# Optimization experiments

Hardware: AMD Instinct MI355X
Metric: run time of the kernel (lower is better)

The kernel has to match this reference:

```python
import jax, jax.numpy as jnp
import numpy as np

N_NODES = 50000
N_EDGES = 800000
K_HOPS = 3


def setup_inputs() -> dict:
    key = jax.random.key(0)
    ks = jax.random.split(key, 8)
    x = jax.random.normal(ks[0], (N_NODES, 56), dtype=jnp.float32)
    edge_index = jax.random.randint(ks[1], (2, N_EDGES), 0, N_NODES, dtype=jnp.int64)
    def glorot(k, shape):
        fan_in, fan_out = shape
        s = (6.0 / (fan_in + fan_out)) ** 0.5
        return jax.random.uniform(k, shape, jnp.float32, -s, s)
    return {
        "x": x,
        "edge_index": edge_index,
        "W1": glorot(ks[2], (56, 64)), "b1": jnp.zeros((64,), jnp.float32),
        "W2": glorot(ks[3], (64, 64)), "b2": jnp.zeros((64,), jnp.float32),
        "W3": glorot(ks[4], (64, 64)), "b3": jnp.zeros((64,), jnp.float32),
        "W4": glorot(ks[5], (64, 256)), "b4": jnp.zeros((256,), jnp.float32),
    }


def _gcn_norm(edge_index, num_nodes, dtype):
    # add self loops (PyG SGConv default), then symmetric D^{-1/2}(A+I)D^{-1/2} weights
    loop = jnp.arange(num_nodes, dtype=edge_index.dtype)
    src = jnp.concatenate([edge_index[0], loop])
    dst = jnp.concatenate([edge_index[1], loop])
    deg = jax.ops.segment_sum(jnp.ones_like(src, dtype=dtype), dst, num_segments=num_nodes)
    dinv = jnp.where(deg > 0, jax.lax.rsqrt(deg), 0.0).astype(dtype)
    norm = dinv[src] * dinv[dst]  # [E + N]
    return src, dst, norm


def _propagate_k(h, src, dst, norm, num_nodes, k):
    # k hops of sparse gather-scale-scatter: h <- A_hat @ h
    for _ in range(k):
        h = jax.ops.segment_sum(h[src] * norm[:, None], dst, num_segments=num_nodes)
    return h


def reference(x, edge_index, W1, b1, W2, b2, W3, b3, W4, b4):
    n = x.shape[0]
    src, dst, norm = _gcn_norm(edge_index, n, x.dtype)
    # SGConv layers (dropout is identity in eval mode)
    h = _propagate_k(x, src, dst, norm, n, K_HOPS) @ W1 + b1
    h = _propagate_k(h, src, dst, norm, n, K_HOPS) @ W2 + b2
    h = _propagate_k(h, src, dst, norm, n, K_HOPS) @ W3 + b3
    return h @ W4 + b4  # [N, output]
```

## Files before the change

### kernel.cpp

```cpp
#include <hip/hip_runtime.h>

#define N_NODES 50000
#define N_EDGES 800000
#define F_IN 56
#define F_PAD 64
#define F_OUT 256
#define NB 32
#define ELL_W 64
#define SEG_SZ 6250


__global__ __launch_bounds__(256) void k_fill(const int* __restrict__ ei,
                                              int* __restrict__ cnt,
                                              int* __restrict__ ell) {
  int seg = blockIdx.x & 7;
  int chunk = blockIdx.x >> 3;
  int nchunks = gridDim.x >> 3;
  int stride = nchunks * blockDim.x;
  for (int e = chunk * blockDim.x + threadIdx.x; e < N_EDGES; e += stride) {
    int d = ei[N_EDGES + e];
    if (d / SEG_SZ == seg) {
      int s = ei[e];
      int pos = atomicAdd(&cnt[d], 1);
      ell[(d << 6) + pos] = s;
    }
  }
}


__global__ void k_dinv(const int* __restrict__ cnt, float* __restrict__ dinv,
                       int* __restrict__ deg, int* __restrict__ ell) {
  int i = blockIdx.x * blockDim.x + threadIdx.x;
  if (i >= N_NODES) return;
  int c = cnt[i];
  dinv[i] = rsqrtf((float)(c + 1));
  deg[i] = c + 1;
  ell[(i << 6) + c] = i;
}


__global__ void k_loadx(const float* __restrict__ x, float* __restrict__ h) {
  int i = blockIdx.x * blockDim.x + threadIdx.x;
  int nn = i >> 6, f = i & 63;
  float v = 0.f;
  if (f < F_IN) v = x[nn * F_IN + f];
  else if (f == F_IN) v = 1.f;
  h[i] = v;
}


__global__ __launch_bounds__(256) void k_hop(const float* __restrict__ hin,
                                             float* __restrict__ hout,
                                             const int* __restrict__ deg,
                                             const int* __restrict__ ell,
                                             const float* __restrict__ dinv,
                                             float* __restrict__ vsave) {
  int node = (blockIdx.x * blockDim.x + threadIdx.x) >> 6;
  int lane = threadIdx.x & 63;
  int d = __builtin_amdgcn_readfirstlane(deg[node]);
  int rec = ell[((size_t)node << 6) + lane];
  rec = (lane < d) ? rec : node;
  float dn = __int_as_float(__builtin_amdgcn_readfirstlane(
      __float_as_int(dinv[node])));
  float wl = (lane < d) ? dinv[rec] * dn : 0.f;

  int sub = lane >> 4;
  int fo  = (lane & 15) << 2;
  float4 acc = make_float4(0.f, 0.f, 0.f, 0.f);

  int ngroups = (d + 3) >> 2;
  int g = 0;
  for (; g + 4 <= ngroups; g += 4) {
    int   s0 = __shfl(rec, g * 4 + sub);
    float w0 = __shfl(wl,  g * 4 + sub);
    int   s1 = __shfl(rec, g * 4 + 4 + sub);
    float w1 = __shfl(wl,  g * 4 + 4 + sub);
    int   s2 = __shfl(rec, g * 4 + 8 + sub);
    float w2 = __shfl(wl,  g * 4 + 8 + sub);
    int   s3 = __shfl(rec, g * 4 + 12 + sub);
    float w3 = __shfl(wl,  g * 4 + 12 + sub);
    float4 a0 = *(const float4*)(hin + (((size_t)s0) << 6) + fo);
    float4 a1 = *(const float4*)(hin + (((size_t)s1) << 6) + fo);
    float4 a2 = *(const float4*)(hin + (((size_t)s2) << 6) + fo);
    float4 a3 = *(const float4*)(hin + (((size_t)s3) << 6) + fo);
    acc.x = fmaf(w0, a0.x, acc.x); acc.y = fmaf(w0, a0.y, acc.y);
    acc.z = fmaf(w0, a0.z, acc.z); acc.w = fmaf(w0, a0.w, acc.w);
    acc.x = fmaf(w1, a1.x, acc.x); acc.y = fmaf(w1, a1.y, acc.y);
    acc.z = fmaf(w1, a1.z, acc.z); acc.w = fmaf(w1, a1.w, acc.w);
    acc.x = fmaf(w2, a2.x, acc.x); acc.y = fmaf(w2, a2.y, acc.y);
    acc.z = fmaf(w2, a2.z, acc.z); acc.w = fmaf(w2, a2.w, acc.w);
    acc.x = fmaf(w3, a3.x, acc.x); acc.y = fmaf(w3, a3.y, acc.y);
    acc.z = fmaf(w3, a3.z, acc.z); acc.w = fmaf(w3, a3.w, acc.w);
  }
  for (; g < ngroups; ++g) {
    int   s0 = __shfl(rec, g * 4 + sub);
    float w0 = __shfl(wl,  g * 4 + sub);
    float4 a0 = *(const float4*)(hin + (((size_t)s0) << 6) + fo);
    acc.x = fmaf(w0, a0.x, acc.x); acc.y = fmaf(w0, a0.y, acc.y);
    acc.z = fmaf(w0, a0.z, acc.z); acc.w = fmaf(w0, a0.w, acc.w);
  }
  acc.x += __shfl_xor(acc.x, 16);
  acc.y += __shfl_xor(acc.y, 16);
  acc.z += __shfl_xor(acc.z, 16);
  acc.w += __shfl_xor(acc.w, 16);
  acc.x += __shfl_xor(acc.x, 32);
  acc.y += __shfl_xor(acc.y, 32);
  acc.z += __shfl_xor(acc.z, 32);
  acc.w += __shfl_xor(acc.w, 32);

  if (lane < 16) {
    *(float4*)(hout + ((size_t)node << 6) + fo) = acc;
  }
  if (vsave != nullptr && lane == 14) vsave[node] = acc.x;
}


__global__ void k_weights(const float* __restrict__ W1, const float* __restrict__ b1,
                          const float* __restrict__ W2, const float* __restrict__ b2,
                          const float* __restrict__ W3, const float* __restrict__ b3,
                          const float* __restrict__ W4, const float* __restrict__ b4,
                          float* __restrict__ Mw, float* __restrict__ c1,
                          float* __restrict__ c2, float* __restrict__ c3) {
  __shared__ float t1[64], t2[64], t3[64];
  int m = blockIdx.x, tid = threadIdx.x;
  if (m < F_IN) {
    if (tid < 64) {
      float a = 0.f;
      for (int k = 0; k < 64; ++k) a = fmaf(W1[m * 64 + k], W2[k * 64 + tid], a);
      t1[tid] = a;
    }
    __syncthreads();
    if (tid < 64) {
      float a = 0.f;
      for (int k = 0; k < 64; ++k) a = fmaf(t1[k], W3[k * 64 + tid], a);
      t2[tid] = a;
    }
    __syncthreads();
    {
      float a = 0.f;
      for (int k = 0; k < 64; ++k) a = fmaf(t2[k], W4[k * 256 + tid], a);
      Mw[m * 256 + tid] = a;
    }
  } else {
    if (tid < 64) {
      float a = 0.f;
      for (int k = 0; k < 64; ++k) a = fmaf(b1[k], W2[k * 64 + tid], a);
      t1[tid] = a;
    }
    __syncthreads();
    if (tid < 64) {
      float a = 0.f, b = 0.f;
      for (int k = 0; k < 64; ++k) {
        float w3 = W3[k * 64 + tid];
        a = fmaf(t1[k], w3, a);
        b = fmaf(b2[k], w3, b);
      }
      t2[tid] = a; t3[tid] = b;
    }
    __syncthreads();
    {
      float a = 0.f, b = 0.f, c = 0.f;
      for (int k = 0; k < 64; ++k) {
        float w4 = W4[k * 256 + tid];
        a = fmaf(t2[k], w4, a);
        b = fmaf(t3[k], w4, b);
        c = fmaf(b3[k], w4, c);
      }
      c1[tid] = a; c2[tid] = b; c3[tid] = c + b4[tid];
    }
  }
}


__global__ __launch_bounds__(256) void k_final(const float* __restrict__ y,
                                               const float* __restrict__ v3,
                                               const float* __restrict__ v6,
                                               const float* __restrict__ Mw,
                                               const float* __restrict__ c1,
                                               const float* __restrict__ c2,
                                               const float* __restrict__ c3,
                                               float* __restrict__ out) {
  __shared__ float4 yl[NB][16];
  __shared__ float v3l[NB], v6l[NB];
  int tid = threadIdx.x;
  int j = tid;

  float4 Mreg[14];
#pragma unroll
  for (int k4 = 0; k4 < 14; ++k4) {
    Mreg[k4].x = Mw[(k4 * 4 + 0) * F_OUT + j];
    Mreg[k4].y = Mw[(k4 * 4 + 1) * F_OUT + j];
    Mreg[k4].z = Mw[(k4 * 4 + 2) * F_OUT + j];
    Mreg[k4].w = Mw[(k4 * 4 + 3) * F_OUT + j];
  }
  float C1 = c1[j], C2 = c2[j], C3 = c3[j];

  int n0 = blockIdx.x * NB;
  int lim = min(NB, N_NODES - n0);
  for (int i = tid; i < lim * 16; i += 256) {
    int nn = i >> 4, q = i & 15;
    yl[nn][q] = *(const float4*)(y + ((size_t)(n0 + nn) << 6) + q * 4);
  }
  if (tid < lim) { v3l[tid] = v3[n0 + tid]; v6l[tid] = v6[n0 + tid]; }
  __syncthreads();

  for (int nn = 0; nn < lim; nn += 2) {
    bool two = (nn + 1) < lim;
    float a0 = fmaf(v6l[nn], C1, fmaf(v3l[nn], C2, C3));
    float a1 = 0.f, a2 = 0.f, a3 = 0.f;
    int nn2 = two ? nn + 1 : nn;
    float b0 = fmaf(v6l[nn2], C1, fmaf(v3l[nn2], C2, C3));
    float b1v = 0.f, b2v = 0.f, b3v = 0.f;
#pragma unroll
    for (int k4 = 0; k4 < 14; ++k4) {
      float4 ya = yl[nn][k4];
      float4 yb = yl[nn2][k4];
      a0  = fmaf(ya.x, Mreg[k4].x, a0);
      a1  = fmaf(ya.y, Mreg[k4].y, a1);
      a2  = fmaf(ya.z, Mreg[k4].z, a2);
      a3  = fmaf(ya.w, Mreg[k4].w, a3);
      b0  = fmaf(yb.x, Mreg[k4].x, b0);
      b1v = fmaf(yb.y, Mreg[k4].y, b1v);
      b2v = fmaf(yb.z, Mreg[k4].z, b2v);
      b3v = fmaf(yb.w, Mreg[k4].w, b3v);
    }
    out[(size_t)(n0 + nn) * F_OUT + j] = (a0 + a1) + (a2 + a3);
    if (two) out[(size_t)(n0 + nn + 1) * F_OUT + j] = (b0 + b1v) + (b2v + b3v);
  }
}


extern "C" void kernel_launch(void* const* d_in, const int* in_sizes, int n_in,
                              void* d_out, int out_size, void* d_ws, size_t ws_size,
                              hipStream_t stream) {
  const float* x  = (const float*)d_in[0];
  const int*   ei = (const int*)d_in[1];
  const float* W1 = (const float*)d_in[2];
  const float* b1 = (const float*)d_in[3];
  const float* W2 = (const float*)d_in[4];
  const float* b2 = (const float*)d_in[5];
  const float* W3 = (const float*)d_in[6];
  const float* b3 = (const float*)d_in[7];
  const float* W4 = (const float*)d_in[8];
  const float* b4 = (const float*)d_in[9];
  float* out = (float*)d_out;

  char* ws = (char*)d_ws;
  size_t off = 0;
  auto take = [&](size_t bytes) -> void* {
    void* p = ws + off;
    off += (bytes + 255) & ~(size_t)255;
    return p;
  };
  int*   cnt   = (int*)take((size_t)N_NODES * 4);
  int*   deg   = (int*)take((size_t)N_NODES * 4);
  float* dinv  = (float*)take((size_t)N_NODES * 4);
  float* v3    = (float*)take((size_t)N_NODES * 4);
  float* v6    = (float*)take((size_t)N_NODES * 4);
  int*   ell   = (int*)take((size_t)N_NODES * ELL_W * 4);
  float* hA    = (float*)take((size_t)N_NODES * F_PAD * 4);
  float* hB    = (float*)take((size_t)N_NODES * F_PAD * 4);
  float* Mw    = (float*)take((size_t)F_IN * F_OUT * 4);
  float* c1    = (float*)take((size_t)F_OUT * 4);
  float* c2    = (float*)take((size_t)F_OUT * 4);
  float* c3    = (float*)take((size_t)F_OUT * 4);

  (void)hipMemsetAsync(cnt, 0, (size_t)N_NODES * 4, stream);
  k_fill<<<1024, 256, 0, stream>>>(ei, cnt, ell);
  k_dinv<<<(N_NODES + 255) / 256, 256, 0, stream>>>(cnt, dinv, deg, ell);
  k_loadx<<<(N_NODES * F_PAD) / 256, 256, 0, stream>>>(x, hA);
  k_weights<<<F_IN + 1, 256, 0, stream>>>(W1, b1, W2, b2, W3, b3, W4, b4, Mw, c1, c2, c3);

  float* src = hA;
  float* dst = hB;
  for (int hop = 1; hop <= 9; ++hop) {
    float* vs = (hop == 3) ? v3 : (hop == 6) ? v6 : nullptr;
    k_hop<<<(N_NODES * F_PAD) / 256, 256, 0, stream>>>(src, dst, deg, ell, dinv, vs);
    float* t = src; src = dst; dst = t;
  }
  k_final<<<(N_NODES + NB - 1) / NB, 256, 0, stream>>>(src, v3, v6, Mw, c1, c2, c3, out);
}
```

Baseline: 398.4 us.

## Fold symmetric normalization into per-node scaling to drop per-edge weights

Rewrites D^{-1/2}(A+I)D^{-1/2} propagation on the scaled variable u = D^{-1/2}h, so each hop becomes an unweighted neighbor sum followed by one multiply by 1/deg. This removes the per-edge dinv[rec] gather and the weight shuffles from the hot hop kernel. Padding lanes now point at an added zero row instead of carrying a zero weight. The final kernel rescales by sqrt(deg) when loading, and its two-node unrolling is removed. The cost is extra per-node arrays and two small memsets.

Measured after the change: 363.3 us. 8.8% less time.

```diff
diff --git a/kernel.cpp b/kernel.cpp
--- a/kernel.cpp
+++ b/kernel.cpp
@@ -8,6 +8,7 @@
 #define NB 32
 #define ELL_W 64
 #define SEG_SZ 6250
+#define ZROW N_NODES
 
 
 __global__ __launch_bounds__(256) void k_fill(const int* __restrict__ ei,
@@ -28,23 +29,29 @@
 }
 
 
-__global__ void k_dinv(const int* __restrict__ cnt, float* __restrict__ dinv,
+__global__ void k_prep(const int* __restrict__ cnt, float* __restrict__ dinv,
+                       float* __restrict__ ideg, float* __restrict__ sqd,
                        int* __restrict__ deg, int* __restrict__ ell) {
   int i = blockIdx.x * blockDim.x + threadIdx.x;
   if (i >= N_NODES) return;
-  int c = cnt[i];
-  dinv[i] = rsqrtf((float)(c + 1));
-  deg[i] = c + 1;
-  ell[(i << 6) + c] = i;
-}
-
-
-__global__ void k_loadx(const float* __restrict__ x, float* __restrict__ h) {
+  int c = cnt[i] + 1;
+  float fc = (float)c;
+  dinv[i] = rsqrtf(fc);
+  ideg[i] = 1.0f / fc;
+  sqd[i]  = sqrtf(fc);
+  deg[i] = c;
+  ell[(i << 6) + (c - 1)] = i;
+}
+
+
+__global__ void k_loadx(const float* __restrict__ x, const float* __restrict__ dinv,
+                        float* __restrict__ h) {
   int i = blockIdx.x * blockDim.x + threadIdx.x;
   int nn = i >> 6, f = i & 63;
+  float di = dinv[nn];
   float v = 0.f;
-  if (f < F_IN) v = x[nn * F_IN + f];
-  else if (f == F_IN) v = 1.f;
+  if (f < F_IN) v = x[nn * F_IN + f] * di;
+  else if (f == F_IN) v = di;
   h[i] = v;
 }
 
@@ -53,16 +60,15 @@
                                              float* __restrict__ hout,
                                              const int* __restrict__ deg,
                                              const int* __restrict__ ell,
-                                             const float* __restrict__ dinv,
+                                             const float* __restrict__ ideg,
                                              float* __restrict__ vsave) {
   int node = (blockIdx.x * blockDim.x + threadIdx.x) >> 6;
   int lane = threadIdx.x & 63;
   int d = __builtin_amdgcn_readfirstlane(deg[node]);
   int rec = ell[((size_t)node << 6) + lane];
-  rec = (lane < d) ? rec : node;
-  float dn = __int_as_float(__builtin_amdgcn_readfirstlane(
-      __float_as_int(dinv[node])));
-  float wl = (lane < d) ? dinv[rec] * dn : 0.f;
+  rec = (lane < d) ? rec : ZROW;
+  float idg = __int_as_float(__builtin_amdgcn_readfirstlane(
+      __float_as_int(ideg[node])));
 
   int sub = lane >> 4;
   int fo  = (lane & 15) << 2;
@@ -71,33 +77,23 @@
   int ngroups = (d + 3) >> 2;
   int g = 0;
   for (; g + 4 <= ngroups; g += 4) {
-    int   s0 = __shfl(rec, g * 4 + sub);
-    float w0 = __shfl(wl,  g * 4 + sub);
-    int   s1 = __shfl(rec, g * 4 + 4 + sub);
-    float w1 = __shfl(wl,  g * 4 + 4 + sub);
-    int   s2 = __shfl(rec, g * 4 + 8 + sub);
-    float w2 = __shfl(wl,  g * 4 + 8 + sub);
-    int   s3 = __shfl(rec, g * 4 + 12 + sub);
-    float w3 = __shfl(wl,  g * 4 + 12 + sub);
+    int s0 = __shfl(rec, g * 4 + sub);
+    int s1 = __shfl(rec, g * 4 + 4 + sub);
+    int s2 = __shfl(rec, g * 4 + 8 + sub);
+    int s3 = __shfl(rec, g * 4 + 12 + sub);
     float4 a0 = *(const float4*)(hin + (((size_t)s0) << 6) + fo);
     float4 a1 = *(const float4*)(hin + (((size_t)s1) << 6) + fo);
     float4 a2 = *(const float4*)(hin + (((size_t)s2) << 6) + fo);
     float4 a3 = *(const float4*)(hin + (((size_t)s3) << 6) + fo);
-    acc.x = fmaf(w0, a0.x, acc.x); acc.y = fmaf(w0, a0.y, acc.y);
-    acc.z = fmaf(w0, a0.z, acc.z); acc.w = fmaf(w0, a0.w, acc.w);
-    acc.x = fmaf(w1, a1.x, acc.x); acc.y = fmaf(w1, a1.y, acc.y);
-    acc.z = fmaf(w1, a1.z, acc.z); acc.w = fmaf(w1, a1.w, acc.w);
-    acc.x = fmaf(w2, a2.x, acc.x); acc.y = fmaf(w2, a2.y, acc.y);
-    acc.z = fmaf(w2, a2.z, acc.z); acc.w = fmaf(w2, a2.w, acc.w);
-    acc.x = fmaf(w3, a3.x, acc.x); acc.y = fmaf(w3, a3.y, acc.y);
-    acc.z = fmaf(w3, a3.z, acc.z); acc.w = fmaf(w3, a3.w, acc.w);
+    acc.x += (a0.x + a1.x) + (a2.x + a3.x);
+    acc.y += (a0.y + a1.y) + (a2.y + a3.y);
+    acc.z += (a0.z + a1.z) + (a2.z + a3.z);
+    acc.w += (a0.w + a1.w) + (a2.w + a3.w);
   }
   for (; g < ngroups; ++g) {
-    int   s0 = __shfl(rec, g * 4 + sub);
-    float w0 = __shfl(wl,  g * 4 + sub);
+    int s0 = __shfl(rec, g * 4 + sub);
     float4 a0 = *(const float4*)(hin + (((size_t)s0) << 6) + fo);
-    acc.x = fmaf(w0, a0.x, acc.x); acc.y = fmaf(w0, a0.y, acc.y);
-    acc.z = fmaf(w0, a0.z, acc.z); acc.w = fmaf(w0, a0.w, acc.w);
+    acc.x += a0.x; acc.y += a0.y; acc.z += a0.z; acc.w += a0.w;
   }
   acc.x += __shfl_xor(acc.x, 16);
   acc.y += __shfl_xor(acc.y, 16);
@@ -107,6 +103,8 @@
   acc.y += __shfl_xor(acc.y, 32);
   acc.z += __shfl_xor(acc.z, 32);
   acc.w += __shfl_xor(acc.w, 32);
+
+  acc.x *= idg; acc.y *= idg; acc.z *= idg; acc.w *= idg;
 
   if (lane < 16) {
     *(float4*)(hout + ((size_t)node << 6) + fo) = acc;
@@ -173,8 +171,9 @@
 
 
 __global__ __launch_bounds__(256) void k_final(const float* __restrict__ y,
-                                               const float* __restrict__ v3,
-                                               const float* __restrict__ v6,
+                                               const float* __restrict__ v3u,
+                                               const float* __restrict__ v6u,
+                                               const float* __restrict__ sqd,
                                                const float* __restrict__ Mw,
                                                const float* __restrict__ c1,
                                                const float* __restrict__ c2,
@@ -199,33 +198,30 @@
   int lim = min(NB, N_NODES - n0);
   for (int i = tid; i < lim * 16; i += 256) {
     int nn = i >> 4, q = i & 15;
-    yl[nn][q] = *(const float4*)(y + ((size_t)(n0 + nn) << 6) + q * 4);
-  }
-  if (tid < lim) { v3l[tid] = v3[n0 + tid]; v6l[tid] = v6[n0 + tid]; }
+    float sq = sqd[n0 + nn];
+    float4 v = *(const float4*)(y + ((size_t)(n0 + nn) << 6) + q * 4);
+    v.x *= sq; v.y *= sq; v.z *= sq; v.w *= sq;
+    yl[nn][q] = v;
+  }
+  if (tid < lim) {
+    float sq = sqd[n0 + tid];
+    v3l[tid] = v3u[n0 + tid] * sq;
+    v6l[tid] = v6u[n0 + tid] * sq;
+  }
   __syncthreads();
 
-  for (int nn = 0; nn < lim; nn += 2) {
-    bool two = (nn + 1) < lim;
+  for (int nn = 0; nn < lim; ++nn) {
     float a0 = fmaf(v6l[nn], C1, fmaf(v3l[nn], C2, C3));
     float a1 = 0.f, a2 = 0.f, a3 = 0.f;
-    int nn2 = two ? nn + 1 : nn;
-    float b0 = fmaf(v6l[nn2], C1, fmaf(v3l[nn2], C2, C3));
-    float b1v = 0.f, b2v = 0.f, b3v = 0.f;
 #pragma unroll
     for (int k4 = 0; k4 < 14; ++k4) {
-      float4 ya = yl[nn][k4];
-      float4 yb = yl[nn2][k4];
-      a0  = fmaf(ya.x, Mreg[k4].x, a0);
-      a1  = fmaf(ya.y, Mreg[k4].y, a1);
-      a2  = fmaf(ya.z, Mreg[k4].z, a2);
-      a3  = fmaf(ya.w, Mreg[k4].w, a3);
-      b0  = fmaf(yb.x, Mreg[k4].x, b0);
-      b1v = fmaf(yb.y, Mreg[k4].y, b1v);
-      b2v = fmaf(yb.z, Mreg[k4].z, b2v);
-      b3v = fmaf(yb.w, Mreg[k4].w, b3v);
+      float4 yv = yl[nn][k4];
+      a0 = fmaf(yv.x, Mreg[k4].x, a0);
+      a1 = fmaf(yv.y, Mreg[k4].y, a1);
+      a2 = fmaf(yv.z, Mreg[k4].z, a2);
+      a3 = fmaf(yv.w, Mreg[k4].w, a3);
     }
     out[(size_t)(n0 + nn) * F_OUT + j] = (a0 + a1) + (a2 + a3);
-    if (two) out[(size_t)(n0 + nn + 1) * F_OUT + j] = (b0 + b1v) + (b2v + b3v);
   }
 }
 
@@ -255,28 +251,32 @@
   int*   cnt   = (int*)take((size_t)N_NODES * 4);
   int*   deg   = (int*)take((size_t)N_NODES * 4);
   float* dinv  = (float*)take((size_t)N_NODES * 4);
+  float* ideg  = (float*)take((size_t)N_NODES * 4);
+  float* sqd   = (float*)take((size_t)N_NODES * 4);
   float* v3    = (float*)take((size_t)N_NODES * 4);
   float* v6    = (float*)take((size_t)N_NODES * 4);
   int*   ell   = (int*)take((size_t)N_NODES * ELL_W * 4);
-  float* hA    = (float*)take((size_t)N_NODES * F_PAD * 4);
-  float* hB    = (float*)take((size_t)N_NODES * F_PAD * 4);
+  float* hA    = (float*)take((size_t)(N_NODES + 1) * F_PAD * 4);
+  float* hB    = (float*)take((size_t)(N_NODES + 1) * F_PAD * 4);
   float* Mw    = (float*)take((size_t)F_IN * F_OUT * 4);
   float* c1    = (float*)take((size_t)F_OUT * 4);
   float* c2    = (float*)take((size_t)F_OUT * 4);
   float* c3    = (float*)take((size_t)F_OUT * 4);
 
   (void)hipMemsetAsync(cnt, 0, (size_t)N_NODES * 4, stream);
+  (void)hipMemsetAsync(hA + (size_t)ZROW * F_PAD, 0, F_PAD * 4, stream);
+  (void)hipMemsetAsync(hB + (size_t)ZROW * F_PAD, 0, F_PAD * 4, stream);
   k_fill<<<1024, 256, 0, stream>>>(ei, cnt, ell);
-  k_dinv<<<(N_NODES + 255) / 256, 256, 0, stream>>>(cnt, dinv, deg, ell);
-  k_loadx<<<(N_NODES * F_PAD) / 256, 256, 0, stream>>>(x, hA);
+  k_prep<<<(N_NODES + 255) / 256, 256, 0, stream>>>(cnt, dinv, ideg, sqd, deg, ell);
+  k_loadx<<<(N_NODES * F_PAD) / 256, 256, 0, stream>>>(x, dinv, hA);
   k_weights<<<F_IN + 1, 256, 0, stream>>>(W1, b1, W2, b2, W3, b3, W4, b4, Mw, c1, c2, c3);
 
   float* src = hA;
   float* dst = hB;
   for (int hop = 1; hop <= 9; ++hop) {
     float* vs = (hop == 3) ? v3 : (hop == 6) ? v6 : nullptr;
-    k_hop<<<(N_NODES * F_PAD) / 256, 256, 0, stream>>>(src, dst, deg, ell, dinv, vs);
+    k_hop<<<(N_NODES * F_PAD) / 256, 256, 0, stream>>>(src, dst, deg, ell, ideg, vs);
     float* t = src; src = dst; dst = t;
   }
-  k_final<<<(N_NODES + NB - 1) / NB, 256, 0, stream>>>(src, v3, v6, Mw, c1, c2, c3, out);
-}
+  k_final<<<(N_NODES + NB - 1) / NB, 256, 0, stream>>>(src, v3, v6, sqd, Mw, c1, c2, c3, out);
+}
```
